# Performance work log

Hardware: AMD Instinct MI355X
Metric: run time of the kernel (lower is better)

The kernel has to match this reference:

```python
import jax, jax.numpy as jnp
import numpy as np

N = 30000      # nodes
E = 1000000    # edges
G = 256        # graphs
IN = 3         # in_channels
H = 8          # heads
D = 16         # per-head dim
HID = 128      # hidden_dim = H*D
L = 3          # num_layers
KP = 17        # num_keypoints
KPE = 16       # kp_emb_dim
NEG = 0.2      # GATv2 leaky_relu negative slope
EPS = 1e-5     # BatchNorm eps


def setup_inputs() -> dict:
    key = jax.random.key(0)
    ks = jax.random.split(key, 24)
    x = jax.random.normal(ks[0], (N, IN), jnp.float32)
    edge_index = jax.random.randint(ks[1], (2, E), 0, N, jnp.int32)
    batch = jnp.sort(jax.random.randint(ks[2], (N,), 0, G, jnp.int32))
    s_in = 1.0 / np.sqrt(IN + KPE)
    s_h = 1.0 / np.sqrt(HID)
    return {
        "x": x,
        "edge_index": edge_index,
        "batch": batch,
        "kp_emb": jax.random.normal(ks[3], (KP, KPE), jnp.float32),
        "w_in": jax.random.normal(ks[4], (IN + KPE, HID), jnp.float32) * s_in,
        "b_in": jax.random.normal(ks[5], (HID,), jnp.float32) * 0.01,
        "w_l": jax.random.normal(ks[6], (L, HID, HID), jnp.float32) * s_h,
        "w_r": jax.random.normal(ks[7], (L, HID, HID), jnp.float32) * s_h,
        "att": jax.random.normal(ks[8], (L, H, D), jnp.float32) * (1.0 / np.sqrt(D)),
        "conv_bias": jax.random.normal(ks[9], (L, HID), jnp.float32) * 0.01,
        "bn_gamma": jnp.ones((L, HID), jnp.float32) + 0.1 * jax.random.normal(ks[10], (L, HID), jnp.float32),
        "bn_beta": 0.1 * jax.random.normal(ks[11], (L, HID), jnp.float32),
        "bn_mean": 0.1 * jax.random.normal(ks[12], (L, HID), jnp.float32),
        "bn_var": 0.5 + jax.random.uniform(ks[13], (L, HID), jnp.float32),
        "w1": jax.random.normal(ks[14], (HID, 2 * HID), jnp.float32) * s_h,
        "b1": jnp.zeros((2 * HID,), jnp.float32),
        "w2": jax.random.normal(ks[15], (2 * HID, HID), jnp.float32) * (1.0 / np.sqrt(2 * HID)),
        "b2": jnp.zeros((HID,), jnp.float32),
        "w3": jax.random.normal(ks[16], (HID, 2), jnp.float32) * s_h,
        "b3": jnp.zeros((2,), jnp.float32),
    }


def reference(x, edge_index, batch, kp_emb, w_in, b_in, w_l, w_r, att, conv_bias,
              bn_gamma, bn_beta, bn_mean, bn_var, w1, b1, w2, b2, w3, b3):
    n = x.shape[0]
    # keypoint id embedding concat + input projection
    kp_ids = jnp.arange(n) % KP
    h = jnp.concatenate([x, kp_emb[kp_ids]], axis=-1) @ w_in + b_in  # [N, HID]
    # GATv2Conv adds self loops by default
    loops = jnp.arange(n, dtype=edge_index.dtype)
    src = jnp.concatenate([edge_index[0], loops])  # message sources (j)
    dst = jnp.concatenate([edge_index[1], loops])  # message targets (i)
    for l in range(L):
        xl = (h @ w_l[l]).reshape(n, H, D)  # source transform (lin_l)
        xr = (h @ w_r[l]).reshape(n, H, D)  # target transform (lin_r)
        z = xl[src] + xr[dst]                              # [Et, H, D]
        score = jnp.einsum('ehd,hd->eh', jax.nn.leaky_relu(z, NEG), att[l])
        # segment softmax over incoming edges of each dst node
        m = jax.ops.segment_max(score, dst, num_segments=n)
        ex = jnp.exp(score - m[dst])
        denom = jax.ops.segment_sum(ex, dst, num_segments=n)
        alpha = ex / denom[dst]                            # [Et, H]
        msg = xl[src] * alpha[..., None]                   # [Et, H, D]
        out = jax.ops.segment_sum(msg, dst, num_segments=n).reshape(n, HID) + conv_bias[l]
        out = jax.nn.relu(out)
        # BatchNorm1d (eval mode: running stats)
        out = (out - bn_mean[l]) * (bn_gamma[l] / jnp.sqrt(bn_var[l] + EPS)) + bn_beta[l]
        h = h + out  # residual (dropout = identity in eval)
    # global mean pool per graph
    sums = jax.ops.segment_sum(h, batch, num_segments=G)
    cnt = jax.ops.segment_sum(jnp.ones((n, 1), h.dtype), batch, num_segments=G)
    g = sums / jnp.maximum(cnt, 1.0)
    # classifier MLP
    g = jax.nn.elu(g @ w1 + b1)
    g = jax.nn.elu(g @ w2 + b2)
    return g @ w3 + b3  # [G, 2]
```

## Files before the change

kernel.cpp:

```cpp
#include <hip/hip_runtime.h>
#include <hip/hip_bf16.h>

#define N_NODES 30000
#define N_EDGES 1000000
#define N_GRAPHS 256
#define HEADS 8
#define DHEAD 16
#define HIDDEN 128
#define LAYERS 3
#define KPN 17
#define KPE 16
#define NEG_SLOPE 0.2f
#define BN_EPS 1e-5f
#define ET (N_EDGES + N_NODES)
#define NBIN 235
#define BINW 128
#define BINCAP 6144
#define CHUNK 4096

typedef __attribute__((ext_vector_type(8))) short bf16x8;
typedef __attribute__((ext_vector_type(4))) float f32x4;

__device__ __forceinline__ unsigned bf16_rne(float f) {
    unsigned u = __float_as_uint(f);
    return (u + 0x7fffu + ((u >> 16) & 1u)) >> 16;
}

__global__ __launch_bounds__(256) void k_bin(const int* __restrict__ ei,
                                             int* __restrict__ bcnt,
                                             unsigned* __restrict__ bdata) {
    __shared__ int lcnt[NBIN];
    __shared__ int lbase[NBIN];
    int base = blockIdx.x * CHUNK;
    int n = N_EDGES - base; if (n > CHUNK) n = CHUNK;
    for (int i = threadIdx.x; i < NBIN; i += 256) lcnt[i] = 0;
    __syncthreads();
    for (int t = threadIdx.x; t < n; t += 256) {
        int d = ei[N_EDGES + base + t];
        atomicAdd(&lcnt[d >> 7], 1);
    }
    __syncthreads();
    for (int i = threadIdx.x; i < NBIN; i += 256) {
        int c = lcnt[i];
        lbase[i] = c ? atomicAdd(&bcnt[i], c) : 0;
        lcnt[i] = 0;
    }
    __syncthreads();
    for (int t = threadIdx.x; t < n; t += 256) {
        int s = ei[base + t];
        int d = ei[N_EDGES + base + t];
        int b = d >> 7;
        int pos = lbase[b] + atomicAdd(&lcnt[b], 1);
        bdata[(size_t)b * BINCAP + pos] = (unsigned)s | ((unsigned)(d & 127) << 15);
    }
}

__global__ __launch_bounds__(256) void k_bscan(const int* __restrict__ bcnt,
                                               int* __restrict__ bbase,
                                               int* __restrict__ ptr) {
    __shared__ int v[256];
    int t = threadIdx.x;
    int c = 0;
    if (t < NBIN) {
        int nodes = N_NODES - t * BINW; if (nodes > BINW) nodes = BINW;
        c = bcnt[t] + nodes;
    }
    v[t] = c;
    __syncthreads();
    for (int off = 1; off < 256; off <<= 1) {
        int x = (t >= off) ? v[t - off] : 0;
        __syncthreads();
        v[t] += x;
        __syncthreads();
    }
    if (t < NBIN) bbase[t] = v[t] - c;
    if (t == 0) ptr[N_NODES] = ET;
}

__global__ __launch_bounds__(256) void k_place2(const int* __restrict__ bcnt,
                                                const unsigned* __restrict__ bdata,
                                                const int* __restrict__ bbase,
                                                int* __restrict__ ptr,
                                                unsigned short* __restrict__ csr_src) {
    __shared__ int hist[BINW];
    __shared__ int pre[BINW];
    __shared__ int nodestart[BINW];
    __shared__ int lofs[BINW];
    int b = blockIdx.x;
    int tid = threadIdx.x;
    int nNodes = N_NODES - b * BINW; if (nNodes > BINW) nNodes = BINW;
    int n = bcnt[b];
    if (tid < BINW) hist[tid] = (tid < nNodes) ? 1 : 0;
    __syncthreads();
    for (int t = tid; t < n; t += 256)
        atomicAdd(&hist[(bdata[(size_t)b * BINCAP + t] >> 15) & 127], 1);
    __syncthreads();
    if (tid < BINW) pre[tid] = hist[tid];
    __syncthreads();
    for (int off = 1; off < BINW; off <<= 1) {
        int x = (tid >= off && tid < BINW) ? pre[tid - off] : 0;
        __syncthreads();
        if (tid < BINW) pre[tid] += x;
        __syncthreads();
    }
    if (tid < BINW) {
        int ns = bbase[b] + pre[tid] - hist[tid];
        nodestart[tid] = ns;
        if (tid < nNodes) {
            int node = b * BINW + tid;
            ptr[node] = ns;
            csr_src[ns] = (unsigned short)node;
        }
        lofs[tid] = 1;
    }
    __syncthreads();
    for (int t = tid; t < n; t += 256) {
        unsigned e = bdata[(size_t)b * BINCAP + t];
        int dl = (e >> 15) & 127;
        int pos = nodestart[dl] + atomicAdd(&lofs[dl], 1);
        csr_src[pos] = (unsigned short)(e & 0x7fffu);
    }
}

__global__ void k_gptr(const int* __restrict__ batch, int* __restrict__ gptr) {
    int g = blockIdx.x * 256 + threadIdx.x;
    if (g > N_GRAPHS) return;
    if (g == N_GRAPHS) { gptr[g] = N_NODES; return; }
    int lo = 0, hi = N_NODES;
    while (lo < hi) {
        int mid = (lo + hi) >> 1;
        if (batch[mid] < g) lo = mid + 1; else hi = mid;
    }
    gptr[g] = lo;
}

__global__ void k_wconv(const float* __restrict__ w_l, const float* __restrict__ w_r,
                        unsigned short* __restrict__ wT) {
    int t = blockIdx.x * 256 + threadIdx.x;
    if (t >= LAYERS * 256 * 128) return;
    int l = t / (256 * 128);
    int rem = t - l * 256 * 128;
    int c = rem >> 7;
    int k = rem & 127;
    float v = (c < 128) ? w_l[(size_t)l * 16384 + k * 128 + c]
                        : w_r[(size_t)l * 16384 + k * 128 + (c - 128)];
    wT[t] = (unsigned short)bf16_rne(v);
}

__global__ void k_inproj(const float* __restrict__ x, const float* __restrict__ kp_emb,
                         const float* __restrict__ w_in, const float* __restrict__ b_in,
                         float* __restrict__ h, unsigned short* __restrict__ hb) {
    int t = blockIdx.x * 256 + threadIdx.x;
    if (t >= N_NODES * HIDDEN) return;
    int c = t & 127, i = t >> 7;
    float acc = b_in[c];
    const float* xi = x + i * 3;
    acc += xi[0] * w_in[0 * 128 + c];
    acc += xi[1] * w_in[1 * 128 + c];
    acc += xi[2] * w_in[2 * 128 + c];
    const float* kp = kp_emb + (i % KPN) * KPE;
#pragma unroll
    for (int k = 0; k < KPE; ++k) acc += kp[k] * w_in[(3 + k) * 128 + c];
    h[t] = acc;
    hb[t] = (unsigned short)bf16_rne(acc);
}

__global__ __launch_bounds__(256) void k_gemm(const unsigned short* __restrict__ hb,
                                              const unsigned short* __restrict__ wT,
                                              unsigned short* __restrict__ xlb,
                                              unsigned short* __restrict__ xrb) {
    int wave = threadIdx.x >> 6;
    int lane = threadIdx.x & 63;
    int brow = blockIdx.x * 32;
    int lr = lane & 15;
    int lk = lane >> 4;
    int ar0 = brow + lr;
    int ar1 = brow + 16 + lr;
    int ar0c = ar0 < N_NODES ? ar0 : N_NODES - 1;
    int ar1c = ar1 < N_NODES ? ar1 : N_NODES - 1;
    int c0 = wave * 64 + lr;

    const unsigned short* ha0 = hb + (size_t)ar0c * 128 + lk * 8;
    const unsigned short* ha1 = hb + (size_t)ar1c * 128 + lk * 8;
    const unsigned short* wb  = wT + (size_t)c0 * 128 + lk * 8;

    f32x4 acc[2][4];
#pragma unroll
    for (int m = 0; m < 2; ++m)
#pragma unroll
        for (int n = 0; n < 4; ++n) acc[m][n] = (f32x4){0.f, 0.f, 0.f, 0.f};

#pragma unroll
    for (int ks = 0; ks < 4; ++ks) {
        bf16x8 a0 = *(const bf16x8*)(ha0 + ks * 32);
        bf16x8 a1 = *(const bf16x8*)(ha1 + ks * 32);
#pragma unroll
        for (int nt = 0; nt < 4; ++nt) {
            bf16x8 b = *(const bf16x8*)(wb + nt * 16 * 128 + ks * 32);
            acc[0][nt] = __builtin_amdgcn_mfma_f32_16x16x32_bf16(a0, b, acc[0][nt], 0, 0, 0);
            acc[1][nt] = __builtin_amdgcn_mfma_f32_16x16x32_bf16(a1, b, acc[1][nt], 0, 0, 0);
        }
    }

    int drow0 = brow + lk * 4;
#pragma unroll
    for (int mt = 0; mt < 2; ++mt) {
#pragma unroll
        for (int nt = 0; nt < 4; ++nt) {
            int col = c0 + nt * 16;
#pragma unroll
            for (int j = 0; j < 4; ++j) {
                int grow = drow0 + mt * 16 + j;
                if (grow >= N_NODES) continue;
                unsigned short bv = (unsigned short)bf16_rne(acc[mt][nt][j]);
                if (col < 128) xlb[(size_t)grow * 128 + col] = bv;
                else           xrb[(size_t)grow * 128 + (col - 128)] = bv;
            }
        }
    }
}

__global__ __launch_bounds__(256) void k_gat(const uint4* __restrict__ xlb4,
                                             const uint4* __restrict__ xrb4,
                                             const int* __restrict__ ptr,
                                             const unsigned short* __restrict__ csr_src,
                                             const float* __restrict__ att_l,
                                             const float* __restrict__ bias_l,
                                             const float* __restrict__ gamma_l,
                                             const float* __restrict__ beta_l,
                                             const float* __restrict__ mean_l,
                                             const float* __restrict__ var_l,
                                             float* __restrict__ h,
                                             unsigned short* __restrict__ hb) {
    int wid = (blockIdx.x * 256 + threadIdx.x) >> 6;
    int lane = threadIdx.x & 63;
    if (wid >= N_NODES) return;
    int i = wid;
    int e4 = lane >> 4;
    int l16 = lane & 15;
    int d0 = 8 * l16;

    uint4 xw = xrb4[(size_t)i * 16 + l16];
    float xr0 = __uint_as_float(xw.x << 16), xr1 = __uint_as_float(xw.x & 0xffff0000u);
    float xr2 = __uint_as_float(xw.y << 16), xr3 = __uint_as_float(xw.y & 0xffff0000u);
    float xr4 = __uint_as_float(xw.z << 16), xr5 = __uint_as_float(xw.z & 0xffff0000u);
    float xr6 = __uint_as_float(xw.w << 16), xr7 = __uint_as_float(xw.w & 0xffff0000u);
    const float L2E = 1.44269504089f;
    float4 avA = *(const float4*)(att_l + d0);
    float4 avB = *(const float4*)(att_l + d0 + 4);
    avA.x *= L2E; avA.y *= L2E; avA.z *= L2E; avA.w *= L2E;
    avB.x *= L2E; avB.y *= L2E; avB.z *= L2E; avB.w *= L2E;
    int e0 = ptr[i], e1 = ptr[i + 1];

    float denom = 0.f;
    float a0 = 0.f, a1 = 0.f, a2 = 0.f, a3 = 0.f, a4 = 0.f, a5 = 0.f, a6 = 0.f, a7 = 0.f;

#define LDQ(KQ, WREG, VREG) { \
    int eo = 4 * (KQ) + e4; \
    int sr = __shfl(sv, eo); \
    VREG = eo < cnt; \
    int rw = VREG ? sr : 0; \
    WREG = xlb4[(size_t)rw * 16 + l16]; \
}
#define PROCQ(WREG, VREG) { \
    float v0 = __uint_as_float(WREG.x << 16), v1 = __uint_as_float(WREG.x & 0xffff0000u); \
    float v2 = __uint_as_float(WREG.y << 16), v3 = __uint_as_float(WREG.y & 0xffff0000u); \
    float v4 = __uint_as_float(WREG.z << 16), v5 = __uint_as_float(WREG.z & 0xffff0000u); \
    float v6 = __uint_as_float(WREG.w << 16), v7 = __uint_as_float(WREG.w & 0xffff0000u); \
    float z0 = v0 + xr0, z1 = v1 + xr1, z2 = v2 + xr2, z3 = v3 + xr3; \
    float z4 = v4 + xr4, z5 = v5 + xr5, z6 = v6 + xr6, z7 = v7 + xr7; \
    z0 = fmaxf(z0, NEG_SLOPE * z0); z1 = fmaxf(z1, NEG_SLOPE * z1); \
    z2 = fmaxf(z2, NEG_SLOPE * z2); z3 = fmaxf(z3, NEG_SLOPE * z3); \
    z4 = fmaxf(z4, NEG_SLOPE * z4); z5 = fmaxf(z5, NEG_SLOPE * z5); \
    z6 = fmaxf(z6, NEG_SLOPE * z6); z7 = fmaxf(z7, NEG_SLOPE * z7); \
    float p = z0 * avA.x + z1 * avA.y + z2 * avA.z + z3 * avA.w \
            + z4 * avB.x + z5 * avB.y + z6 * avB.z + z7 * avB.w; \
    p += __shfl_xor(p, 1); \
    float ex = VREG ? exp2f(p) : 0.f; \
    denom += ex; \
    a0 += ex * v0; a1 += ex * v1; a2 += ex * v2; a3 += ex * v3; \
    a4 += ex * v4; a5 += ex * v5; a6 += ex * v6; a7 += ex * v7; \
}

    for (int base = e0; base < e1; base += 64) {
        int idx = base + lane;
        int sv = (idx < e1) ? (int)csr_src[idx] : 0;
        int cnt = e1 - base; if (cnt > 64) cnt = 64;
        int nq = (cnt + 3) >> 2;

        uint4 w0, w1; bool b0 = false, b1 = false;
        LDQ(0, w0, b0);
        if (1 < nq) LDQ(1, w1, b1);
        int k = 0;
        for (; k + 2 < nq; k += 2) {
            uint4 n0, n1; bool c0v, c1v;
            LDQ(k + 2, n0, c0v);
            LDQ(k + 3, n1, c1v);
            PROCQ(w0, b0); PROCQ(w1, b1);
            w0 = n0; b0 = c0v; w1 = n1; b1 = c1v;
        }
        PROCQ(w0, b0);
        if (k + 1 < nq) PROCQ(w1, b1);
    }
#undef LDQ
#undef PROCQ

    denom += __shfl_xor(denom, 16); denom += __shfl_xor(denom, 32);
    a0 += __shfl_xor(a0, 16); a0 += __shfl_xor(a0, 32);
    a1 += __shfl_xor(a1, 16); a1 += __shfl_xor(a1, 32);
    a2 += __shfl_xor(a2, 16); a2 += __shfl_xor(a2, 32);
    a3 += __shfl_xor(a3, 16); a3 += __shfl_xor(a3, 32);
    a4 += __shfl_xor(a4, 16); a4 += __shfl_xor(a4, 32);
    a5 += __shfl_xor(a5, 16); a5 += __shfl_xor(a5, 32);
    a6 += __shfl_xor(a6, 16); a6 += __shfl_xor(a6, 32);
    a7 += __shfl_xor(a7, 16); a7 += __shfl_xor(a7, 32);

    if (e4 == 0) {
        float inv = 1.f / denom;
        float4 biaA = *(const float4*)(bias_l + d0),  biaB = *(const float4*)(bias_l + d0 + 4);
        float4 gamA = *(const float4*)(gamma_l + d0), gamB = *(const float4*)(gamma_l + d0 + 4);
        float4 betA = *(const float4*)(beta_l + d0),  betB = *(const float4*)(beta_l + d0 + 4);
        float4 meaA = *(const float4*)(mean_l + d0),  meaB = *(const float4*)(mean_l + d0 + 4);
        float4 varA = *(const float4*)(var_l + d0),   varB = *(const float4*)(var_l + d0 + 4);
        float o0 = fmaxf(a0 * inv + biaA.x, 0.f);
        float o1 = fmaxf(a1 * inv + biaA.y, 0.f);
        float o2 = fmaxf(a2 * inv + biaA.z, 0.f);
        float o3 = fmaxf(a3 * inv + biaA.w, 0.f);
        float o4 = fmaxf(a4 * inv + biaB.x, 0.f);
        float o5 = fmaxf(a5 * inv + biaB.y, 0.f);
        float o6 = fmaxf(a6 * inv + biaB.z, 0.f);
        float o7 = fmaxf(a7 * inv + biaB.w, 0.f);
        o0 = (o0 - meaA.x) * (gamA.x * rsqrtf(varA.x + BN_EPS)) + betA.x;
        o1 = (o1 - meaA.y) * (gamA.y * rsqrtf(varA.y + BN_EPS)) + betA.y;
        o2 = (o2 - meaA.z) * (gamA.z * rsqrtf(varA.z + BN_EPS)) + betA.z;
        o3 = (o3 - meaA.w) * (gamA.w * rsqrtf(varA.w + BN_EPS)) + betA.w;
        o4 = (o4 - meaB.x) * (gamB.x * rsqrtf(varB.x + BN_EPS)) + betB.x;
        o5 = (o5 - meaB.y) * (gamB.y * rsqrtf(varB.y + BN_EPS)) + betB.y;
        o6 = (o6 - meaB.z) * (gamB.z * rsqrtf(varB.z + BN_EPS)) + betB.z;
        o7 = (o7 - meaB.w) * (gamB.w * rsqrtf(varB.w + BN_EPS)) + betB.w;
        float4 hvA = *(const float4*)(h + (size_t)i * 128 + d0);
        float4 hvB = *(const float4*)(h + (size_t)i * 128 + d0 + 4);
        hvA.x += o0; hvA.y += o1; hvA.z += o2; hvA.w += o3;
        hvB.x += o4; hvB.y += o5; hvB.z += o6; hvB.w += o7;
        *(float4*)(h + (size_t)i * 128 + d0) = hvA;
        *(float4*)(h + (size_t)i * 128 + d0 + 4) = hvB;
        uint4 pk;
        pk.x = bf16_rne(hvA.x) | (bf16_rne(hvA.y) << 16);
        pk.y = bf16_rne(hvA.z) | (bf16_rne(hvA.w) << 16);
        pk.z = bf16_rne(hvB.x) | (bf16_rne(hvB.y) << 16);
        pk.w = bf16_rne(hvB.z) | (bf16_rne(hvB.w) << 16);
        *(uint4*)(hb + (size_t)i * 128 + d0) = pk;
    }
}

__global__ __launch_bounds__(256) void k_poolmlp(const float* __restrict__ h,
                                                 const int* __restrict__ gptr,
                                                 const float* __restrict__ w1, const float* __restrict__ b1,
                                                 const float* __restrict__ w2, const float* __restrict__ b2,
                                                 const float* __restrict__ w3, const float* __restrict__ b3,
                                                 float* __restrict__ out) {
    __shared__ float red[256];
    __shared__ float g[128], t1[256], t2[128];
    int b = blockIdx.x, t = threadIdx.x;
    int c = t & 127, half = t >> 7;
    int lo = gptr[b], hi = gptr[b + 1];
    float s = 0.f;
    for (int i = lo + half; i < hi; i += 2) s += h[(size_t)i * 128 + c];
    red[t] = s;
    __syncthreads();
    if (half == 0) {
        float cntf = fmaxf((float)(hi - lo), 1.0f);
        g[c] = (red[c] + red[c + 128]) / cntf;
    }
    __syncthreads();
    {
        float acc = b1[t];
        for (int k = 0; k < 128; ++k) acc += g[k] * w1[k * 256 + t];
        t1[t] = acc > 0.f ? acc : expm1f(acc);
    }
    __syncthreads();
    if (t < 128) {
        float acc = b2[t];
        for (int k = 0; k < 256; ++k) acc += t1[k] * w2[k * 128 + t];
        t2[t] = acc > 0.f ? acc : expm1f(acc);
    }
    __syncthreads();
    if (t < 2) {
        float acc = b3[t];
        for (int k = 0; k < 128; ++k) acc += t2[k] * w3[k * 2 + t];
        out[b * 2 + t] = acc;
    }
}

extern "C" void kernel_launch(void* const* d_in, const int* in_sizes, int n_in,
                              void* d_out, int out_size, void* d_ws, size_t ws_size,
                              hipStream_t stream) {
    const float* x        = (const float*)d_in[0];
    const int*   ei       = (const int*)d_in[1];
    const int*   batch    = (const int*)d_in[2];
    const float* kp_emb   = (const float*)d_in[3];
    const float* w_in     = (const float*)d_in[4];
    const float* b_in     = (const float*)d_in[5];
    const float* w_l      = (const float*)d_in[6];
    const float* w_r      = (const float*)d_in[7];
    const float* att      = (const float*)d_in[8];
    const float* conv_b   = (const float*)d_in[9];
    const float* bn_gamma = (const float*)d_in[10];
    const float* bn_beta  = (const float*)d_in[11];
    const float* bn_mean  = (const float*)d_in[12];
    const float* bn_var   = (const float*)d_in[13];
    const float* w1 = (const float*)d_in[14];
    const float* b1 = (const float*)d_in[15];
    const float* w2 = (const float*)d_in[16];
    const float* b2 = (const float*)d_in[17];
    const float* w3 = (const float*)d_in[18];
    const float* b3 = (const float*)d_in[19];
    float* out = (float*)d_out;

    char* ws = (char*)d_ws;
    const size_t OFF_H    = 0;
    const size_t OFF_HB   = OFF_H    + 15360000;
    const size_t OFF_XL   = OFF_HB   + 7680000;
    const size_t OFF_XR   = OFF_XL   + 7680000;
    const size_t OFF_WT   = OFF_XR   + 7680000;
    const size_t OFF_PTR  = OFF_WT   + 196608;
    const size_t OFF_BCNT = OFF_PTR  + 120320;
    const size_t OFF_BBAS = OFF_BCNT + 1024;
    const size_t OFF_SRC  = OFF_BBAS + 1024;
    const size_t OFF_GPTR = OFF_SRC  + 2060032;

    float*          h      = (float*)(ws + OFF_H);
    unsigned short* hb     = (unsigned short*)(ws + OFF_HB);
    unsigned short* xlb    = (unsigned short*)(ws + OFF_XL);
    unsigned short* xrb    = (unsigned short*)(ws + OFF_XR);
    unsigned*       bdata  = (unsigned*)(ws + OFF_XR);
    unsigned short* wT     = (unsigned short*)(ws + OFF_WT);
    int*            ptr    = (int*)(ws + OFF_PTR);
    int*            bcnt   = (int*)(ws + OFF_BCNT);
    int*            bbase  = (int*)(ws + OFF_BBAS);
    unsigned short* csrsrc = (unsigned short*)(ws + OFF_SRC);
    int*            gptr   = (int*)(ws + OFF_GPTR);

    hipMemsetAsync(bcnt, 0, NBIN * 4, stream);
    k_bin<<<(N_EDGES + CHUNK - 1) / CHUNK, 256, 0, stream>>>(ei, bcnt, bdata);
    k_bscan<<<1, 256, 0, stream>>>(bcnt, bbase, ptr);
    k_place2<<<NBIN, 256, 0, stream>>>(bcnt, bdata, bbase, ptr, csrsrc);
    k_gptr<<<2, 256, 0, stream>>>(batch, gptr);
    k_wconv<<<(LAYERS * 256 * 128 + 255) / 256, 256, 0, stream>>>(w_l, w_r, wT);

    k_inproj<<<(N_NODES * 128 + 255) / 256, 256, 0, stream>>>(x, kp_emb, w_in, b_in, h, hb);

    for (int l = 0; l < LAYERS; ++l) {
        k_gemm<<<(N_NODES + 31) / 32, 256, 0, stream>>>(hb, wT + (size_t)l * 256 * 128, xlb, xrb);
        k_gat<<<(N_NODES + 3) / 4, 256, 0, stream>>>(
            (const uint4*)xlb, (const uint4*)xrb, ptr, csrsrc,
            att + (size_t)l * 128, conv_b + (size_t)l * 128,
            bn_gamma + (size_t)l * 128, bn_beta + (size_t)l * 128,
            bn_mean + (size_t)l * 128, bn_var + (size_t)l * 128, h, hb);
    }

    k_poolmlp<<<N_GRAPHS, 256, 0, stream>>>(h, gptr, w1, b1, w2, b2, w3, b3, out);
}
```

Baseline: 282.3 us.

## Merge setup kernels and rewrite GAT leaky-relu score as abs-based packed FMAs

Folds the bin scan, graph-pointer search and weight conversion into one auxiliary launch, removing two kernel launches from the setup path. In the GAT edge loop, leaky_relu(z)·a is rewritten as 0.6·z·a + 0.4·|z|·a, with the slope factors folded into precomputed attention vectors. This removes the per-element max and multiply and arranges the work as float2 FMA pairs so the compiler can emit packed math. The accumulators are likewise restructured into float2 FMAs. The algebraic rewrite changes rounding slightly and adds a few extra registers.

```diff
diff --git a/kernel.cpp b/kernel.cpp
--- a/kernel.cpp
+++ b/kernel.cpp
@@ -55,26 +55,55 @@
     }
 }
 
-__global__ __launch_bounds__(256) void k_bscan(const int* __restrict__ bcnt,
-                                               int* __restrict__ bbase,
-                                               int* __restrict__ ptr) {
-    __shared__ int v[256];
+__global__ __launch_bounds__(256) void k_aux(const int* __restrict__ bcnt,
+                                             const int* __restrict__ batch,
+                                             const float* __restrict__ w_l,
+                                             const float* __restrict__ w_r,
+                                             int* __restrict__ bbase,
+                                             int* __restrict__ ptr,
+                                             int* __restrict__ gptr,
+                                             unsigned short* __restrict__ wT) {
     int t = threadIdx.x;
-    int c = 0;
-    if (t < NBIN) {
-        int nodes = N_NODES - t * BINW; if (nodes > BINW) nodes = BINW;
-        c = bcnt[t] + nodes;
-    }
-    v[t] = c;
-    __syncthreads();
-    for (int off = 1; off < 256; off <<= 1) {
-        int x = (t >= off) ? v[t - off] : 0;
+    if (blockIdx.x == 0) {
+        for (int g = t; g <= N_GRAPHS; g += 256) {
+            if (g == N_GRAPHS) { gptr[g] = N_NODES; }
+            else {
+                int lo = 0, hi = N_NODES;
+                while (lo < hi) {
+                    int mid = (lo + hi) >> 1;
+                    if (batch[mid] < g) lo = mid + 1; else hi = mid;
+                }
+                gptr[g] = lo;
+            }
+        }
+        __shared__ int v[256];
+        int c = 0;
+        if (t < NBIN) {
+            int nodes = N_NODES - t * BINW; if (nodes > BINW) nodes = BINW;
+            c = bcnt[t] + nodes;
+        }
+        v[t] = c;
         __syncthreads();
-        v[t] += x;
-        __syncthreads();
-    }
-    if (t < NBIN) bbase[t] = v[t] - c;
-    if (t == 0) ptr[N_NODES] = ET;
+        for (int off = 1; off < 256; off <<= 1) {
+            int x = (t >= off) ? v[t - off] : 0;
+            __syncthreads();
+            v[t] += x;
+            __syncthreads();
+        }
+        if (t < NBIN) bbase[t] = v[t] - c;
+        if (t == 0) ptr[N_NODES] = ET;
+    } else {
+        int idx = (blockIdx.x - 1) * 256 + t;
+        if (idx < LAYERS * 256 * 128) {
+            int l = idx / (256 * 128);
+            int rem = idx - l * 256 * 128;
+            int c = rem >> 7;
+            int k = rem & 127;
+            float v = (c < 128) ? w_l[(size_t)l * 16384 + k * 128 + c]
+                                : w_r[(size_t)l * 16384 + k * 128 + (c - 128)];
+            wT[idx] = (unsigned short)bf16_rne(v);
+        }
+    }
 }
 
 __global__ __launch_bounds__(256) void k_place2(const int* __restrict__ bcnt,
@@ -120,31 +149,6 @@
         int pos = nodestart[dl] + atomicAdd(&lofs[dl], 1);
         csr_src[pos] = (unsigned short)(e & 0x7fffu);
     }
-}
-
-__global__ void k_gptr(const int* __restrict__ batch, int* __restrict__ gptr) {
-    int g = blockIdx.x * 256 + threadIdx.x;
-    if (g > N_GRAPHS) return;
-    if (g == N_GRAPHS) { gptr[g] = N_NODES; return; }
-    int lo = 0, hi = N_NODES;
-    while (lo < hi) {
-        int mid = (lo + hi) >> 1;
-        if (batch[mid] < g) lo = mid + 1; else hi = mid;
-    }
-    gptr[g] = lo;
-}
-
-__global__ void k_wconv(const float* __restrict__ w_l, const float* __restrict__ w_r,
-                        unsigned short* __restrict__ wT) {
-    int t = blockIdx.x * 256 + threadIdx.x;
-    if (t >= LAYERS * 256 * 128) return;
-    int l = t / (256 * 128);
-    int rem = t - l * 256 * 128;
-    int c = rem >> 7;
-    int k = rem & 127;
-    float v = (c < 128) ? w_l[(size_t)l * 16384 + k * 128 + c]
-                        : w_r[(size_t)l * 16384 + k * 128 + (c - 128)];
-    wT[t] = (unsigned short)bf16_rne(v);
 }
 
 __global__ void k_inproj(const float* __restrict__ x, const float* __restrict__ kp_emb,
@@ -241,19 +245,26 @@
     int d0 = 8 * l16;
 
     uint4 xw = xrb4[(size_t)i * 16 + l16];
-    float xr0 = __uint_as_float(xw.x << 16), xr1 = __uint_as_float(xw.x & 0xffff0000u);
-    float xr2 = __uint_as_float(xw.y << 16), xr3 = __uint_as_float(xw.y & 0xffff0000u);
-    float xr4 = __uint_as_float(xw.z << 16), xr5 = __uint_as_float(xw.z & 0xffff0000u);
-    float xr6 = __uint_as_float(xw.w << 16), xr7 = __uint_as_float(xw.w & 0xffff0000u);
+    float2 xra = make_float2(__uint_as_float(xw.x << 16), __uint_as_float(xw.x & 0xffff0000u));
+    float2 xrb_ = make_float2(__uint_as_float(xw.y << 16), __uint_as_float(xw.y & 0xffff0000u));
+    float2 xrc = make_float2(__uint_as_float(xw.z << 16), __uint_as_float(xw.z & 0xffff0000u));
+    float2 xrd = make_float2(__uint_as_float(xw.w << 16), __uint_as_float(xw.w & 0xffff0000u));
     const float L2E = 1.44269504089f;
     float4 avA = *(const float4*)(att_l + d0);
     float4 avB = *(const float4*)(att_l + d0 + 4);
-    avA.x *= L2E; avA.y *= L2E; avA.z *= L2E; avA.w *= L2E;
-    avB.x *= L2E; avB.y *= L2E; avB.z *= L2E; avB.w *= L2E;
+    float2 a6a = make_float2(avA.x * (0.6f * L2E), avA.y * (0.6f * L2E));
+    float2 a6b = make_float2(avA.z * (0.6f * L2E), avA.w * (0.6f * L2E));
+    float2 a6c = make_float2(avB.x * (0.6f * L2E), avB.y * (0.6f * L2E));
+    float2 a6d = make_float2(avB.z * (0.6f * L2E), avB.w * (0.6f * L2E));
+    float2 a4a = make_float2(avA.x * (0.4f * L2E), avA.y * (0.4f * L2E));
+    float2 a4b = make_float2(avA.z * (0.4f * L2E), avA.w * (0.4f * L2E));
+    float2 a4c = make_float2(avB.x * (0.4f * L2E), avB.y * (0.4f * L2E));
+    float2 a4d = make_float2(avB.z * (0.4f * L2E), avB.w * (0.4f * L2E));
     int e0 = ptr[i], e1 = ptr[i + 1];
 
     float denom = 0.f;
-    float a0 = 0.f, a1 = 0.f, a2 = 0.f, a3 = 0.f, a4 = 0.f, a5 = 0.f, a6 = 0.f, a7 = 0.f;
+    float2 acA = make_float2(0.f, 0.f), acB = make_float2(0.f, 0.f);
+    float2 acC = make_float2(0.f, 0.f), acD = make_float2(0.f, 0.f);
 
 #define LDQ(KQ, WREG, VREG) { \
     int eo = 4 * (KQ) + e4; \
@@ -263,23 +274,32 @@
     WREG = xlb4[(size_t)rw * 16 + l16]; \
 }
 #define PROCQ(WREG, VREG) { \
-    float v0 = __uint_as_float(WREG.x << 16), v1 = __uint_as_float(WREG.x & 0xffff0000u); \
-    float v2 = __uint_as_float(WREG.y << 16), v3 = __uint_as_float(WREG.y & 0xffff0000u); \
-    float v4 = __uint_as_float(WREG.z << 16), v5 = __uint_as_float(WREG.z & 0xffff0000u); \
-    float v6 = __uint_as_float(WREG.w << 16), v7 = __uint_as_float(WREG.w & 0xffff0000u); \
-    float z0 = v0 + xr0, z1 = v1 + xr1, z2 = v2 + xr2, z3 = v3 + xr3; \
-    float z4 = v4 + xr4, z5 = v5 + xr5, z6 = v6 + xr6, z7 = v7 + xr7; \
-    z0 = fmaxf(z0, NEG_SLOPE * z0); z1 = fmaxf(z1, NEG_SLOPE * z1); \
-    z2 = fmaxf(z2, NEG_SLOPE * z2); z3 = fmaxf(z3, NEG_SLOPE * z3); \
-    z4 = fmaxf(z4, NEG_SLOPE * z4); z5 = fmaxf(z5, NEG_SLOPE * z5); \
-    z6 = fmaxf(z6, NEG_SLOPE * z6); z7 = fmaxf(z7, NEG_SLOPE * z7); \
-    float p = z0 * avA.x + z1 * avA.y + z2 * avA.z + z3 * avA.w \
-            + z4 * avB.x + z5 * avB.y + z6 * avB.z + z7 * avB.w; \
+    float2 va = make_float2(__uint_as_float(WREG.x << 16), __uint_as_float(WREG.x & 0xffff0000u)); \
+    float2 vb = make_float2(__uint_as_float(WREG.y << 16), __uint_as_float(WREG.y & 0xffff0000u)); \
+    float2 vc = make_float2(__uint_as_float(WREG.z << 16), __uint_as_float(WREG.z & 0xffff0000u)); \
+    float2 vd = make_float2(__uint_as_float(WREG.w << 16), __uint_as_float(WREG.w & 0xffff0000u)); \
+    float2 za, zb, zc, zd; \
+    za.x = va.x + xra.x;  za.y = va.y + xra.y; \
+    zb.x = vb.x + xrb_.x; zb.y = vb.y + xrb_.y; \
+    zc.x = vc.x + xrc.x;  zc.y = vc.y + xrc.y; \
+    zd.x = vd.x + xrd.x;  zd.y = vd.y + xrd.y; \
+    float2 p6, p4; \
+    p6.x = za.x * a6a.x;  p6.y = za.y * a6a.y; \
+    p6.x = fmaf(zb.x, a6b.x, p6.x); p6.y = fmaf(zb.y, a6b.y, p6.y); \
+    p6.x = fmaf(zc.x, a6c.x, p6.x); p6.y = fmaf(zc.y, a6c.y, p6.y); \
+    p6.x = fmaf(zd.x, a6d.x, p6.x); p6.y = fmaf(zd.y, a6d.y, p6.y); \
+    p4.x = fabsf(za.x) * a4a.x;  p4.y = fabsf(za.y) * a4a.y; \
+    p4.x = fmaf(fabsf(zb.x), a4b.x, p4.x); p4.y = fmaf(fabsf(zb.y), a4b.y, p4.y); \
+    p4.x = fmaf(fabsf(zc.x), a4c.x, p4.x); p4.y = fmaf(fabsf(zc.y), a4c.y, p4.y); \
+    p4.x = fmaf(fabsf(zd.x), a4d.x, p4.x); p4.y = fmaf(fabsf(zd.y), a4d.y, p4.y); \
+    float p = (p6.x + p4.x) + (p6.y + p4.y); \
     p += __shfl_xor(p, 1); \
     float ex = VREG ? exp2f(p) : 0.f; \
     denom += ex; \
-    a0 += ex * v0; a1 += ex * v1; a2 += ex * v2; a3 += ex * v3; \
-    a4 += ex * v4; a5 += ex * v5; a6 += ex * v6; a7 += ex * v7; \
+    acA.x = fmaf(ex, va.x, acA.x); acA.y = fmaf(ex, va.y, acA.y); \
+    acB.x = fmaf(ex, vb.x, acB.x); acB.y = fmaf(ex, vb.y, acB.y); \
+    acC.x = fmaf(ex, vc.x, acC.x); acC.y = fmaf(ex, vc.y, acC.y); \
+    acD.x = fmaf(ex, vd.x, acD.x); acD.y = fmaf(ex, vd.y, acD.y); \
 }
 
     for (int base = e0; base < e1; base += 64) {
@@ -306,14 +326,14 @@
 #undef PROCQ
 
     denom += __shfl_xor(denom, 16); denom += __shfl_xor(denom, 32);
-    a0 += __shfl_xor(a0, 16); a0 += __shfl_xor(a0, 32);
-    a1 += __shfl_xor(a1, 16); a1 += __shfl_xor(a1, 32);
-    a2 += __shfl_xor(a2, 16); a2 += __shfl_xor(a2, 32);
-    a3 += __shfl_xor(a3, 16); a3 += __shfl_xor(a3, 32);
-    a4 += __shfl_xor(a4, 16); a4 += __shfl_xor(a4, 32);
-    a5 += __shfl_xor(a5, 16); a5 += __shfl_xor(a5, 32);
-    a6 += __shfl_xor(a6, 16); a6 += __shfl_xor(a6, 32);
-    a7 += __shfl_xor(a7, 16); a7 += __shfl_xor(a7, 32);
+    acA.x += __shfl_xor(acA.x, 16); acA.x += __shfl_xor(acA.x, 32);
+    acA.y += __shfl_xor(acA.y, 16); acA.y += __shfl_xor(acA.y, 32);
+    acB.x += __shfl_xor(acB.x, 16); acB.x += __shfl_xor(acB.x, 32);
+    acB.y += __shfl_xor(acB.y, 16); acB.y += __shfl_xor(acB.y, 32);
+    acC.x += __shfl_xor(acC.x, 16); acC.x += __shfl_xor(acC.x, 32);
+    acC.y += __shfl_xor(acC.y, 16); acC.y += __shfl_xor(acC.y, 32);
+    acD.x += __shfl_xor(acD.x, 16); acD.x += __shfl_xor(acD.x, 32);
+    acD.y += __shfl_xor(acD.y, 16); acD.y += __shfl_xor(acD.y, 32);
 
     if (e4 == 0) {
         float inv = 1.f / denom;
@@ -322,14 +342,14 @@
         float4 betA = *(const float4*)(beta_l + d0),  betB = *(const float4*)(beta_l + d0 + 4);
         float4 meaA = *(const float4*)(mean_l + d0),  meaB = *(const float4*)(mean_l + d0 + 4);
         float4 varA = *(const float4*)(var_l + d0),   varB = *(const float4*)(var_l + d0 + 4);
-        float o0 = fmaxf(a0 * inv + biaA.x, 0.f);
-        float o1 = fmaxf(a1 * inv + biaA.y, 0.f);
-        float o2 = fmaxf(a2 * inv + biaA.z, 0.f);
-        float o3 = fmaxf(a3 * inv + biaA.w, 0.f);
-        float o4 = fmaxf(a4 * inv + biaB.x, 0.f);
-        float o5 = fmaxf(a5 * inv + biaB.y, 0.f);
-        float o6 = fmaxf(a6 * inv + biaB.z, 0.f);
-        float o7 = fmaxf(a7 * inv + biaB.w, 0.f);
+        float o0 = fmaxf(acA.x * inv + biaA.x, 0.f);
+        float o1 = fmaxf(acA.y * inv + biaA.y, 0.f);
+        float o2 = fmaxf(acB.x * inv + biaA.z, 0.f);
+        float o3 = fmaxf(acB.y * inv + biaA.w, 0.f);
+        float o4 = fmaxf(acC.x * inv + biaB.x, 0.f);
+        float o5 = fmaxf(acC.y * inv + biaB.y, 0.f);
+        float o6 = fmaxf(acD.x * inv + biaB.z, 0.f);
+        float o7 = fmaxf(acD.y * inv + biaB.w, 0.f);
         o0 = (o0 - meaA.x) * (gamA.x * rsqrtf(varA.x + BN_EPS)) + betA.x;
         o1 = (o1 - meaA.y) * (gamA.y * rsqrtf(varA.y + BN_EPS)) + betA.y;
         o2 = (o2 - meaA.z) * (gamA.z * rsqrtf(varA.z + BN_EPS)) + betA.z;
@@ -443,10 +463,9 @@
 
     hipMemsetAsync(bcnt, 0, NBIN * 4, stream);
     k_bin<<<(N_EDGES + CHUNK - 1) / CHUNK, 256, 0, stream>>>(ei, bcnt, bdata);
-    k_bscan<<<1, 256, 0, stream>>>(bcnt, bbase, ptr);
+    k_aux<<<1 + (LAYERS * 256 * 128 + 255) / 256, 256, 0, stream>>>(bcnt, batch, w_l, w_r,
+                                                                    bbase, ptr, gptr, wT);
     k_place2<<<NBIN, 256, 0, stream>>>(bcnt, bdata, bbase, ptr, csrsrc);
-    k_gptr<<<2, 256, 0, stream>>>(batch, gptr);
-    k_wconv<<<(LAYERS * 256 * 128 + 255) / 256, 256, 0, stream>>>(w_l, w_r, wT);
 
     k_inproj<<<(N_NODES * 128 + 255) / 256, 256, 0, stream>>>(x, kp_emb, w_in, b_in, h, hb);
 
```

Result: no change. 280.3 us (-0.7%).
